# Optimization experiments

Measured on AMD Instinct MI355X. Metric: run time of the kernel, lower is better.

## Reference

```python
import jax, jax.numpy as jnp
import numpy as np

HEADS = 12
NUM_IMS = 1
SCALE = 1.0


def _layernorm(x, g, b, eps=1e-5):
    m = jnp.mean(x, axis=-1, keepdims=True)
    v = jnp.var(x, axis=-1, keepdims=True)
    return (x - m) / jnp.sqrt(v + eps) * g + b


def _mha(q, k, v):
    # q: [B, Nq, C], k/v: [B, Nk, C]; multi-head softmax attention
    B, Nq, C = q.shape
    d = C // HEADS
    qh = q.reshape(B, Nq, HEADS, d)
    kh = k.reshape(B, k.shape[1], HEADS, d)
    vh = v.reshape(B, v.shape[1], HEADS, d)
    sim = jnp.einsum('bihd,bjhd->bhij', qh, kh) * (d ** -0.5)
    w = jax.nn.softmax(sim, axis=-1)
    out = jnp.einsum('bhij,bjhd->bihd', w, vh)
    return out.reshape(B, Nq, C)


def _forward(hidden_states, encoder_hidden_states, ln1_g, ln1_b, ln2_g, ln2_b,
             sa_wq, sa_wk, sa_wv, sa_wo, sa_wo_b, ff_ln_g, ff_ln_b, ff_w1, ff_w2,
             alpha_attn, alpha_dense, ca_wq, ca_wk, ca_wv, ca_wo, ca_wo_b):
    B, N, C = hidden_states.shape
    end_pos = encoder_hidden_states.shape[1] - 16 * NUM_IMS
    text = encoder_hidden_states[:, :end_pos]   # [B, Lt, C]
    face = encoder_hidden_states[:, end_pos:]   # [B, 16, C]

    x = hidden_states
    # gated self-attention over visual tokens + face tokens
    x_ln = _layernorm(x, ln1_g, ln1_b)
    face_ln = _layernorm(face, ln1_g, ln1_b)
    comb = jnp.concatenate([x_ln, face_ln], axis=1)  # [B, N+16, C]
    attn_out = _mha(comb @ sa_wq, comb @ sa_wk, comb @ sa_wv) @ sa_wo + sa_wo_b
    attn_out = attn_out[:, :N]
    x = x + SCALE * jnp.tanh(alpha_attn) * attn_out

    # gated GEGLU feed-forward (norm2 outside, FF has its own LayerNorm)
    h = _layernorm(x, ln2_g, ln2_b)
    h = _layernorm(h, ff_ln_g, ff_ln_b)
    h = h @ ff_w1                                 # [B, N, 2*inner]
    a, gate = jnp.split(h, 2, axis=-1)
    h = (a * jax.nn.gelu(gate, approximate=False)) @ ff_w2
    x = x + SCALE * jnp.tanh(alpha_dense) * h

    residual = x
    # cross attention against text tokens (diffusers Attention, residual_connection=True)
    out = _mha(x @ ca_wq, text @ ca_wk, text @ ca_wv) @ ca_wo + ca_wo_b
    return out + residual


def setup_inputs() -> dict:
    key = jax.random.key(0)
    ks = jax.random.split(key, 16)
    B, N, C, L, INNER = 2, 1024, 768, 77 + 16 * NUM_IMS, 3072
    W = 0.02
    return {
        'hidden_states': jax.random.normal(ks[0], (B, N, C), jnp.float32),
        'encoder_hidden_states': jax.random.normal(ks[1], (B, L, C), jnp.float32),
        'ln1_g': jnp.ones((C,), jnp.float32),
        'ln1_b': jnp.zeros((C,), jnp.float32),
        'ln2_g': jnp.ones((C,), jnp.float32),
        'ln2_b': jnp.zeros((C,), jnp.float32),
        'sa_wq': jax.random.normal(ks[2], (C, C), jnp.float32) * W,
        'sa_wk': jax.random.normal(ks[3], (C, C), jnp.float32) * W,
        'sa_wv': jax.random.normal(ks[4], (C, C), jnp.float32) * W,
        'sa_wo': jax.random.normal(ks[5], (C, C), jnp.float32) * W,
        'sa_wo_b': jnp.zeros((C,), jnp.float32),
        'ff_ln_g': jnp.ones((C,), jnp.float32),
        'ff_ln_b': jnp.zeros((C,), jnp.float32),
        'ff_w1': jax.random.normal(ks[6], (C, 2 * INNER), jnp.float32) * W,
        'ff_w2': jax.random.normal(ks[7], (INNER, C), jnp.float32) * W,
        'alpha_attn': jnp.float32(0.5),
        'alpha_dense': jnp.float32(0.5),
        'ca_wq': jax.random.normal(ks[8], (C, C), jnp.float32) * W,
        'ca_wk': jax.random.normal(ks[9], (C, C), jnp.float32) * W,
        'ca_wv': jax.random.normal(ks[10], (C, C), jnp.float32) * W,
        'ca_wo': jax.random.normal(ks[11], (C, C), jnp.float32) * W,
        'ca_wo_b': jnp.zeros((C,), jnp.float32),
    }


def reference(hidden_states, encoder_hidden_states, ln1_g, ln1_b, ln2_g, ln2_b,
              sa_wq, sa_wk, sa_wv, sa_wo, sa_wo_b, ff_ln_g, ff_ln_b, ff_w1, ff_w2,
              alpha_attn, alpha_dense, ca_wq, ca_wk, ca_wv, ca_wo, ca_wo_b):
    return _forward(hidden_states, encoder_hidden_states, ln1_g, ln1_b, ln2_g, ln2_b,
                    sa_wq, sa_wk, sa_wv, sa_wo, sa_wo_b, ff_ln_g, ff_ln_b, ff_w1, ff_w2,
                    alpha_attn, alpha_dense, ca_wq, ca_wk, ca_wv, ca_wo, ca_wo_b)
```

## Files before the change

kernel.cpp:

```cpp
#include <hip/hip_runtime.h>
#include <hip/hip_bf16.h>
#include <math.h>


#define C_DIM 768
#define B_DIM 2
#define N_DIM 1024
#define NC_DIM 1040
#define L_DIM 93
#define TEXT_LEN 77
#define INNER 3072
#define MNX 1572864

typedef unsigned short ushort_t;
typedef __bf16 bf16x8 __attribute__((ext_vector_type(8)));
typedef float f32x4 __attribute__((ext_vector_type(4)));

__device__ __forceinline__ ushort_t f2b(float f) {
  __hip_bfloat16 h = __float2bfloat16(f);
  return *(ushort_t*)&h;
}
__device__ __forceinline__ float b2f(ushort_t u) {
  __hip_bfloat16 h = *(__hip_bfloat16*)&u;
  return __bfloat162float(h);
}

__device__ __forceinline__ void g2lds16(const void* g, void* l) {
  __builtin_amdgcn_global_load_lds(
      (const __attribute__((address_space(1))) unsigned int*)g,
      (__attribute__((address_space(3))) unsigned int*)l, 16, 0, 0);
}

#define WX1    0u
#define WX2    6291456u
#define WQKV   12582912u
#define WBB1   22167552u
#define WG     47333376u
#define WS1    59916288u
#define WTEXT  63062016u
#define WATT2  63298560u
#define WWQKV  66444288u
#define WWO    69983232u
#define WW1    71162880u
#define WW2    80600064u
#define WCAWQ  85318656u
#define WCAKV  86498304u
#define WCAWO  88857600u
#define WVT1   90037248u
#define WVT2   93379584u
#define WOPART WBB1
#define WLBUF  WG
#define WATTN  (WG + 524288u)
#define WPART  WBB1

__device__ __forceinline__ float block_sum(float v, float* sh) {
#pragma unroll
  for (int o = 32; o > 0; o >>= 1) v += __shfl_down(v, o);
  int lane = threadIdx.x & 63, w = threadIdx.x >> 6;
  if (lane == 0) sh[w] = v;
  __syncthreads();
  float r = sh[0] + sh[1] + sh[2] + sh[3];
  __syncthreads();
  return r;
}

struct WtDesc {
  const float* src[10];
  ushort_t*    dst[10];
  int K[10];
  int N[10];
  int tilesX[10];
  int ileave[10];
  int start[11];
};

__global__ __launch_bounds__(256)
void wtrans_batched(WtDesc d) {
  __shared__ float tile[64][65];
  int bid = blockIdx.x;
  int j = 0;
  while (j < 9 && bid >= d.start[j + 1]) ++j;
  int ti = bid - d.start[j];
  int K = d.K[j], N = d.N[j];
  int n0 = (ti % d.tilesX[j]) * 64, k0 = (ti / d.tilesX[j]) * 64;
  const float* in = d.src[j];
  ushort_t* out = d.dst[j];
  int il = d.ileave[j];
  int t = threadIdx.x;
#pragma unroll
  for (int p = 0; p < 16; ++p) {
    int idx = t + p * 256;
    int r = idx >> 6, c = idx & 63;
    tile[r][c] = in[(size_t)(k0 + r) * N + n0 + c];
  }
  __syncthreads();
#pragma unroll
  for (int p = 0; p < 16; ++p) {
    int idx = t + p * 256;
    int r = idx >> 6, c = idx & 63;
    int nrow = n0 + r;
    int dstrow = il ? ((nrow < INNER) ? (nrow * 2) : ((nrow - INNER) * 2 + 1)) : nrow;
    out[(size_t)dstrow * K + k0 + c] = f2b(tile[c][r]);
  }
}

__global__ __launch_bounds__(256)
void ln_concat_kernel(const float* __restrict__ x, const float* __restrict__ enc,
                      const float* __restrict__ g, const float* __restrict__ b,
                      ushort_t* __restrict__ comb) {
  __shared__ float sh[4];
  int r = blockIdx.x;
  int bb = r / NC_DIM, i = r % NC_DIM;
  const float* src = (i < N_DIM)
      ? (x   + ((size_t)bb * N_DIM + i) * C_DIM)
      : (enc + ((size_t)bb * L_DIM + TEXT_LEN + (i - N_DIM)) * C_DIM);
  float v[3];
#pragma unroll
  for (int j = 0; j < 3; ++j) v[j] = src[threadIdx.x + j * 256];
  float mean = block_sum(v[0] + v[1] + v[2], sh) * (1.f / C_DIM);
  float sq = 0.f;
#pragma unroll
  for (int j = 0; j < 3; ++j) { float d = v[j] - mean; sq += d * d; }
  float rstd = rsqrtf(block_sum(sq, sh) * (1.f / C_DIM) + 1e-5f);
  ushort_t* dst = comb + (size_t)r * C_DIM;
#pragma unroll
  for (int j = 0; j < 3; ++j) {
    int c = threadIdx.x + j * 256;
    dst[c] = f2b((v[j] - mean) * rstd * g[c] + b[c]);
  }
}

__global__ __launch_bounds__(256)
void gemm_bf16(const ushort_t* __restrict__ A, const ushort_t* __restrict__ Bt,
               ushort_t* __restrict__ Ob, ushort_t* __restrict__ Og,
               int M, int N, int K) {
  __shared__ ushort_t sA[2][128 * 32];
  __shared__ ushort_t sB[2][128 * 32];
  int t = threadIdx.x;
  int w = t >> 6, ln = t & 63;
  int m0 = blockIdx.y * 128, n0 = blockIdx.x * 128;
  int wm = (w >> 1) * 64, wn = (w & 1) * 64;
  int lr = ln & 15, lq = ln >> 4;
  int seg_r = ln >> 2, seg_c = (ln & 3) * 8;

  f32x4 acc[4][4];
#pragma unroll
  for (int mi = 0; mi < 4; ++mi)
#pragma unroll
    for (int ni = 0; ni < 4; ++ni) acc[mi][ni] = (f32x4){0.f, 0.f, 0.f, 0.f};

#define STAGE(k0_, buf_)                                                     \
  do {                                                                       \
    _Pragma("unroll") for (int l = 0; l < 2; ++l) {                          \
      int s = w * 2 + l;                                                     \
      int arow = m0 + s * 16 + seg_r;                                        \
      arow = arow < M ? arow : M - 1;                                        \
      g2lds16(A + (size_t)arow * K + (k0_) + seg_c, &sA[buf_][s * 512]);     \
      int nrow = n0 + s * 16 + seg_r;                                        \
      g2lds16(Bt + (size_t)nrow * K + (k0_) + seg_c, &sB[buf_][s * 512]);    \
    }                                                                        \
  } while (0)

  STAGE(0, 0);
  __syncthreads();
  int cur = 0;
  for (int k0 = 0; k0 < K; k0 += 32) {
    if (k0 + 32 < K) STAGE(k0 + 32, cur ^ 1);
    bf16x8 af[4], bfr[4];
#pragma unroll
    for (int mi = 0; mi < 4; ++mi)
      af[mi] = *(const bf16x8*)&sA[cur][(wm + mi * 16 + lr) * 32 + lq * 8];
#pragma unroll
    for (int ni = 0; ni < 4; ++ni)
      bfr[ni] = *(const bf16x8*)&sB[cur][(wn + ni * 16 + lr) * 32 + lq * 8];
#pragma unroll
    for (int mi = 0; mi < 4; ++mi)
#pragma unroll
      for (int ni = 0; ni < 4; ++ni)
        acc[mi][ni] = __builtin_amdgcn_mfma_f32_16x16x32_bf16(
            af[mi], bfr[ni], acc[mi][ni], 0, 0, 0);
    __syncthreads();
    cur ^= 1;
  }
#undef STAGE

  if (Og) {
#pragma unroll
    for (int mi = 0; mi < 4; ++mi)
#pragma unroll
      for (int ni = 0; ni < 4; ++ni) {
        int col = n0 + wn + ni * 16 + lr;
#pragma unroll
        for (int r = 0; r < 4; ++r) {
          float val = acc[mi][ni][r];
          float other = __shfl_xor(val, 1);
          if (!(lr & 1)) {
            float a = val, gate = other;
            float ge = 0.5f * gate * (1.f + erff(gate * 0.70710678118654752f));
            int row = m0 + wm + mi * 16 + lq * 4 + r;
            Og[(size_t)row * INNER + (col >> 1)] = f2b(a * ge);
          }
        }
      }
  } else {
#pragma unroll
    for (int mi = 0; mi < 4; ++mi)
#pragma unroll
      for (int ni = 0; ni < 4; ++ni) {
        int col = n0 + wn + ni * 16 + lr;
#pragma unroll
        for (int r = 0; r < 4; ++r) {
          int row = m0 + wm + mi * 16 + lq * 4 + r;
          if (row < M) Ob[(size_t)row * N + col] = f2b(acc[mi][ni][r]);
        }
      }
  }
}

__global__ __launch_bounds__(256)
void gemm64(const ushort_t* __restrict__ A, const ushort_t* __restrict__ Bt,
            float* __restrict__ Out, ushort_t* __restrict__ Ob,
            float* __restrict__ Part,
            int M, int N, int K, int Ksplit,
            const float* __restrict__ bias, const float* __restrict__ res,
            const float* __restrict__ alphaPtr) {
  __shared__ ushort_t sA[2][4096];
  __shared__ ushort_t sB[2][4096];
  int t = threadIdx.x;
  int w = t >> 6, ln = t & 63;
  int m0 = blockIdx.y * 64, n0 = blockIdx.x * 64;
  int wm = (w >> 1) * 32, wn = (w & 1) * 32;
  int lr = ln & 15, lq = ln >> 4;
  int srow = (w & 1) * 32 + (ln >> 2);
  int skoff = (w >> 1) * 32 + (ln & 3) * 8;
  int kbeg = blockIdx.z * Ksplit;
  int kend = kbeg + Ksplit; if (kend > K) kend = K;

  f32x4 acc[2][2];
#pragma unroll
  for (int mi = 0; mi < 2; ++mi)
#pragma unroll
    for (int ni = 0; ni < 2; ++ni) acc[mi][ni] = (f32x4){0.f, 0.f, 0.f, 0.f};

#define STG64(k0_, buf_)                                                      \
  do {                                                                        \
    _Pragma("unroll") for (int i = 0; i < 2; ++i) {                           \
      int ar = m0 + srow + i * 16; ar = ar < M ? ar : M - 1;                  \
      g2lds16(A + (size_t)ar * K + (k0_) + skoff,                             \
              (char*)sA + (buf_) * 8192 + w * 2048 + i * 1024);               \
      int nr = n0 + srow + i * 16;                                            \
      g2lds16(Bt + (size_t)nr * K + (k0_) + skoff,                            \
              (char*)sB + (buf_) * 8192 + w * 2048 + i * 1024);               \
    }                                                                         \
  } while (0)

  STG64(kbeg, 0);
  __syncthreads();
  int cur = 0;
  for (int k0 = kbeg; k0 < kend; k0 += 64) {
    if (k0 + 64 < kend) STG64(k0 + 64, cur ^ 1);
#pragma unroll
    for (int s = 0; s < 2; ++s) {
      bf16x8 a0 = *(const bf16x8*)&sA[cur][s * 2048 + (wm + lr) * 32 + lq * 8];
      bf16x8 a1 = *(const bf16x8*)&sA[cur][s * 2048 + (wm + 16 + lr) * 32 + lq * 8];
      bf16x8 b0 = *(const bf16x8*)&sB[cur][s * 2048 + (wn + lr) * 32 + lq * 8];
      bf16x8 b1 = *(const bf16x8*)&sB[cur][s * 2048 + (wn + 16 + lr) * 32 + lq * 8];
      acc[0][0] = __builtin_amdgcn_mfma_f32_16x16x32_bf16(a0, b0, acc[0][0], 0, 0, 0);
      acc[0][1] = __builtin_amdgcn_mfma_f32_16x16x32_bf16(a0, b1, acc[0][1], 0, 0, 0);
      acc[1][0] = __builtin_amdgcn_mfma_f32_16x16x32_bf16(a1, b0, acc[1][0], 0, 0, 0);
      acc[1][1] = __builtin_amdgcn_mfma_f32_16x16x32_bf16(a1, b1, acc[1][1], 0, 0, 0);
    }
    __syncthreads();
    cur ^= 1;
  }
#undef STG64

  if (Part) {
    float* P = Part + (size_t)blockIdx.z * M * N;
#pragma unroll
    for (int mi = 0; mi < 2; ++mi)
#pragma unroll
      for (int ni = 0; ni < 2; ++ni) {
        int col = n0 + wn + ni * 16 + lr;
#pragma unroll
        for (int r = 0; r < 4; ++r) {
          int row = m0 + wm + mi * 16 + lq * 4 + r;
          if (row < M) P[(size_t)row * N + col] = acc[mi][ni][r];
        }
      }
  } else {
    float f = alphaPtr ? tanhf(alphaPtr[0]) : 1.0f;
#pragma unroll
    for (int mi = 0; mi < 2; ++mi)
#pragma unroll
      for (int ni = 0; ni < 2; ++ni) {
        int col = n0 + wn + ni * 16 + lr;
        float bv = bias ? bias[col] : 0.f;
#pragma unroll
        for (int r = 0; r < 4; ++r) {
          int row = m0 + wm + mi * 16 + lq * 4 + r;
          if (row < M) {
            float val = acc[mi][ni][r] + bv;
            if (res) val = res[(size_t)row * N + col] + f * val;
            if (Out) Out[(size_t)row * N + col] = val;
            if (Ob)  Ob[(size_t)row * N + col] = f2b(val);
          }
        }
      }
  }
}

__global__ __launch_bounds__(256)
void splitk_epi(const float* __restrict__ Part, int nz, float* __restrict__ Out,
                ushort_t* __restrict__ Ob, int MN, int N,
                const float* __restrict__ bias, const float* __restrict__ res,
                const float* __restrict__ alphaPtr) {
  int idx = (blockIdx.x * 256 + threadIdx.x) * 4;
  if (idx >= MN) return;
  float f = alphaPtr ? tanhf(alphaPtr[0]) : 1.0f;
  float v[4] = {0.f, 0.f, 0.f, 0.f};
  for (int z = 0; z < nz; ++z) {
    float4 a = *(const float4*)&Part[(size_t)z * MN + idx];
    v[0] += a.x; v[1] += a.y; v[2] += a.z; v[3] += a.w;
  }
  if (bias) {
    int col = idx % N;
    float4 bb = *(const float4*)&bias[col];
    v[0] += bb.x; v[1] += bb.y; v[2] += bb.z; v[3] += bb.w;
  }
  if (res) {
    float4 rr = *(const float4*)&res[idx];
    v[0] = rr.x + f * v[0]; v[1] = rr.y + f * v[1];
    v[2] = rr.z + f * v[2]; v[3] = rr.w + f * v[3];
  }
  if (Out) *(float4*)&Out[idx] = make_float4(v[0], v[1], v[2], v[3]);
  if (Ob) {
    ushort4 o;
    o.x = f2b(v[0]); o.y = f2b(v[1]); o.z = f2b(v[2]); o.w = f2b(v[3]);
    *(ushort4*)&Ob[idx] = o;
  }
}

__global__ __launch_bounds__(256)
void woepi_ln_kernel(const float* __restrict__ Part, int nz,
                     const float* __restrict__ bias, const float* __restrict__ xres,
                     const float* __restrict__ alphaPtr, float* __restrict__ x1,
                     const float* __restrict__ g1, const float* __restrict__ b1,
                     const float* __restrict__ g2, const float* __restrict__ b2,
                     ushort_t* __restrict__ hh) {
  __shared__ float sh[4];
  int row = blockIdx.x;
  float f = tanhf(alphaPtr[0]);
  float v[3];
#pragma unroll
  for (int j = 0; j < 3; ++j) {
    int c = threadIdx.x + j * 256;
    float s = 0.f;
    for (int z = 0; z < nz; ++z) s += Part[(size_t)z * MNX + (size_t)row * C_DIM + c];
    s += bias[c];
    float xv = xres[(size_t)row * C_DIM + c] + f * s;
    x1[(size_t)row * C_DIM + c] = xv;
    v[j] = xv;
  }
  float mean = block_sum(v[0] + v[1] + v[2], sh) * (1.f / C_DIM);
  float sq = 0.f;
#pragma unroll
  for (int j = 0; j < 3; ++j) { float d = v[j] - mean; sq += d * d; }
  float rstd = rsqrtf(block_sum(sq, sh) * (1.f / C_DIM) + 1e-5f);
  float y[3];
#pragma unroll
  for (int j = 0; j < 3; ++j) {
    int c = threadIdx.x + j * 256;
    y[j] = (v[j] - mean) * rstd * g1[c] + b1[c];
  }
  float mean2 = block_sum(y[0] + y[1] + y[2], sh) * (1.f / C_DIM);
  sq = 0.f;
#pragma unroll
  for (int j = 0; j < 3; ++j) { float d = y[j] - mean2; sq += d * d; }
  float rstd2 = rsqrtf(block_sum(sq, sh) * (1.f / C_DIM) + 1e-5f);
#pragma unroll
  for (int j = 0; j < 3; ++j) {
    int c = threadIdx.x + j * 256;
    hh[(size_t)row * C_DIM + c] = f2b((y[j] - mean2) * rstd2 * g2[c] + b2[c]);
  }
}

__global__ __launch_bounds__(256)
void vtrans_kernel(const ushort_t* __restrict__ V, ushort_t* __restrict__ Vt,
                   int rows_per_b, int stride, int Nk, int Nkp) {
  __shared__ ushort_t tile[64][68];
  int k0 = blockIdx.x * 64;
  int h = blockIdx.y, b = blockIdx.z;
  int t = threadIdx.x;
#pragma unroll
  for (int p = 0; p < 4; ++p) {
    int r = p * 16 + (t >> 4), c = (t & 15) * 4;
    int key = k0 + r;
    ushort4 u = make_ushort4(0, 0, 0, 0);
    if (key < Nk)
      u = *(const ushort4*)&V[((size_t)(b * rows_per_b + key)) * stride + h * 64 + c];
    *(ushort4*)&tile[r][c] = u;
  }
  __syncthreads();
  size_t base = ((size_t)(b * 12 + h)) * 64 * Nkp;
#pragma unroll
  for (int p = 0; p < 4; ++p) {
    int dv = p * 16 + (t >> 4), kc = (t & 15) * 4;
    ushort4 u;
    u.x = tile[kc + 0][dv]; u.y = tile[kc + 1][dv];
    u.z = tile[kc + 2][dv]; u.w = tile[kc + 3][dv];
    *(ushort4*)&Vt[base + (size_t)dv * Nkp + k0 + kc] = u;
  }
}

__global__ __launch_bounds__(256)
void attn_mfma(const ushort_t* __restrict__ Q, const ushort_t* __restrict__ K,
               const ushort_t* __restrict__ Vt, ushort_t* __restrict__ O,
               float* __restrict__ Opart, float* __restrict__ lbuf,
               int q_rows_per_b, int kv_rows_per_b, int Nk, int Nkp,
               int qstride, int kstride, int nchunk) {
  __shared__ ushort_t sQ[4096];
  __shared__ ushort_t sK[2][4096];
  __shared__ ushort_t sV[2][4096];
  __shared__ ushort_t sP[4][1024];
  const float scale = 0.18033688011112042f;
  const float M0 = 16.0f;
  int t = threadIdx.x;
  int w = t >> 6, ln = t & 63;
  int col = ln & 15, quad = ln >> 4;
  int z = blockIdx.z;
  int b = z / nchunk, kc = z % nchunk;
  int h = blockIdx.y, q0 = blockIdx.x * 64;
  size_t vt_base = ((size_t)(b * 12 + h)) * 64 * Nkp;
  int ntiles = Nkp >> 6;
  int t0 = (kc * ntiles) / nchunk;
  int t1 = ((kc + 1) * ntiles) / nchunk;

#define STAGE_KV(kt_, bb_)                                                    \
  do {                                                                        \
    _Pragma("unroll") for (int s = 0; s < 2; ++s) {                           \
      int key = (kt_) * 64 + w * 16 + (ln >> 2);                              \
      g2lds16(K + (size_t)(b * kv_rows_per_b + key) * kstride                 \
                + h * 64 + s * 32 + (ln & 3) * 8,                             \
              (char*)sK[bb_] + s * 4096 + w * 1024);                          \
      int dv = w * 16 + (ln >> 2);                                            \
      g2lds16(Vt + vt_base + (size_t)dv * Nkp                                 \
                + (kt_) * 64 + s * 32 + (ln & 3) * 8,                         \
              (char*)sV[bb_] + s * 4096 + w * 1024);                          \
    }                                                                         \
  } while (0)

#pragma unroll
  for (int s = 0; s < 2; ++s) {
    int r = q0 + w * 16 + (ln >> 2);
    g2lds16(Q + (size_t)(b * q_rows_per_b + r) * qstride + h * 64 + s * 32 + (ln & 3) * 8,
            (char*)sQ + s * 4096 + w * 1024);
  }
  STAGE_KV(t0, 0);
  __syncthreads();
  bf16x8 qa[2];
#pragma unroll
  for (int s = 0; s < 2; ++s)
    qa[s] = *(const bf16x8*)&sQ[s * 2048 + (w * 16 + col) * 32 + quad * 8];

  f32x4 oacc[4];
#pragma unroll
  for (int i = 0; i < 4; ++i) oacc[i] = (f32x4){0.f, 0.f, 0.f, 0.f};
  float l_i[4] = {0.f, 0.f, 0.f, 0.f};

  ushort_t* sPw = sP[w];
  int bb = 0;

  for (int kt = t0; kt < t1; ++kt) {
    if (kt + 1 < t1) STAGE_KV(kt + 1, bb ^ 1);

    f32x4 cs[4];
#pragma unroll
    for (int nblk = 0; nblk < 4; ++nblk) {
      cs[nblk] = (f32x4){0.f, 0.f, 0.f, 0.f};
#pragma unroll
      for (int s = 0; s < 2; ++s) {
        bf16x8 kb = *(const bf16x8*)&sK[bb][s * 2048 + (nblk * 16 + col) * 32 + quad * 8];
        cs[nblk] = __builtin_amdgcn_mfma_f32_16x16x32_bf16(qa[s], kb, cs[nblk], 0, 0, 0);
      }
    }
    if (kt * 64 + 64 > Nk) {
#pragma unroll
      for (int nblk = 0; nblk < 4; ++nblk) {
        bool valid = (kt * 64 + nblk * 16 + col) < Nk;
#pragma unroll
        for (int r = 0; r < 4; ++r)
          cs[nblk][r] = valid ? cs[nblk][r] : -1e30f;
      }
    }
#pragma unroll
    for (int r = 0; r < 4; ++r) {
      int row = quad * 4 + r;
#pragma unroll
      for (int nblk = 0; nblk < 4; ++nblk) {
        float p = exp2f(fmaf(cs[nblk][r], scale, -M0));
        l_i[r] += p;
        int kin = (nblk & 1) * 16 + col;
        sPw[(nblk >> 1) * 512 + row * 32 + (kin ^ (quad << 3))] = f2b(p);
      }
    }
#pragma unroll
    for (int s = 0; s < 2; ++s) {
      bf16x8 pa = *(const bf16x8*)&sPw[s * 512 + col * 32 + ((quad ^ ((col >> 2) & 3)) << 3)];
#pragma unroll
      for (int nblk = 0; nblk < 4; ++nblk) {
        bf16x8 vb = *(const bf16x8*)&sV[bb][s * 2048 + (nblk * 16 + col) * 32 + quad * 8];
        oacc[nblk] = __builtin_amdgcn_mfma_f32_16x16x32_bf16(pa, vb, oacc[nblk], 0, 0, 0);
      }
    }
    if (kt + 1 < t1) __syncthreads();
    bb ^= 1;
  }
#undef STAGE_KV

#pragma unroll
  for (int r = 0; r < 4; ++r) {
    float ps = l_i[r];
#pragma unroll
    for (int o = 1; o < 16; o <<= 1) ps += __shfl_xor(ps, o);
    int qglob = b * N_DIM + q0 + w * 16 + quad * 4 + r;
    if (Opart) {
      if (col == 0) lbuf[(size_t)kc * (B_DIM * N_DIM * 12) + (size_t)qglob * 12 + h] = ps;
      float* op = Opart + (size_t)kc * MNX + (size_t)qglob * C_DIM + h * 64;
#pragma unroll
      for (int nblk = 0; nblk < 4; ++nblk)
        op[nblk * 16 + col] = oacc[nblk][r];
    } else {
      float inv = 1.f / ps;
#pragma unroll
      for (int nblk = 0; nblk < 4; ++nblk)
        O[(size_t)qglob * C_DIM + h * 64 + nblk * 16 + col] = f2b(oacc[nblk][r] * inv);
    }
  }
}

__global__ __launch_bounds__(256)
void attn_merge(const float* __restrict__ Opart, const float* __restrict__ lbuf,
                ushort_t* __restrict__ Ob, int nchunk) {
  int idx = (blockIdx.x * 256 + threadIdx.x) * 4;
  if (idx >= MNX) return;
  int row = idx / C_DIM, c = idx % C_DIM;
  int h = c >> 6;
  float l = 0.f;
  float v[4] = {0.f, 0.f, 0.f, 0.f};
  for (int kc = 0; kc < nchunk; ++kc) {
    l += lbuf[(size_t)kc * (B_DIM * N_DIM * 12) + (size_t)row * 12 + h];
    float4 p = *(const float4*)&Opart[(size_t)kc * MNX + idx];
    v[0] += p.x; v[1] += p.y; v[2] += p.z; v[3] += p.w;
  }
  float inv = 1.f / l;
  ushort4 o;
  o.x = f2b(v[0] * inv); o.y = f2b(v[1] * inv);
  o.z = f2b(v[2] * inv); o.w = f2b(v[3] * inv);
  *(ushort4*)&Ob[idx] = o;
}

__global__ __launch_bounds__(256)
void gather_text_kernel(const float* __restrict__ enc, ushort_t* __restrict__ out) {
  int r = blockIdx.x;
  int bb = r / TEXT_LEN, j = r % TEXT_LEN;
  const float* src = enc + ((size_t)bb * L_DIM + j) * C_DIM;
  ushort_t* dst = out + (size_t)r * C_DIM;
#pragma unroll
  for (int l = 0; l < 3; ++l) {
    int c = threadIdx.x + l * 256;
    dst[c] = f2b(src[c]);
  }
}

extern "C" void kernel_launch(void* const* d_in, const int* in_sizes, int n_in,
                              void* d_out, int out_size, void* d_ws, size_t ws_size,
                              hipStream_t stream) {
  const float* x        = (const float*)d_in[0];
  const float* enc      = (const float*)d_in[1];
  const float* ln1_g    = (const float*)d_in[2];
  const float* ln1_b    = (const float*)d_in[3];
  const float* ln2_g    = (const float*)d_in[4];
  const float* ln2_b    = (const float*)d_in[5];
  const float* sa_wq    = (const float*)d_in[6];
  const float* sa_wk    = (const float*)d_in[7];
  const float* sa_wv    = (const float*)d_in[8];
  const float* sa_wo    = (const float*)d_in[9];
  const float* sa_wo_b  = (const float*)d_in[10];
  const float* ff_ln_g  = (const float*)d_in[11];
  const float* ff_ln_b  = (const float*)d_in[12];
  const float* ff_w1    = (const float*)d_in[13];
  const float* ff_w2    = (const float*)d_in[14];
  const float* a_attn   = (const float*)d_in[15];
  const float* a_dense  = (const float*)d_in[16];
  const float* ca_wq    = (const float*)d_in[17];
  const float* ca_wk    = (const float*)d_in[18];
  const float* ca_wv    = (const float*)d_in[19];
  const float* ca_wo    = (const float*)d_in[20];
  const float* ca_wo_b  = (const float*)d_in[21];

  char* ws = (char*)d_ws;
  float*    x1     = (float*)(ws + WX1);
  float*    x2     = (float*)(ws + WX2);
  ushort_t* qkv_b  = (ushort_t*)(ws + WQKV);
  ushort_t* q2b    = (ushort_t*)(ws + WQKV);
  ushort_t* kv2b   = (ushort_t*)(ws + WQKV + 3145728u);
  ushort_t* comb_b = (ushort_t*)(ws + WBB1);
  float*    opart  = (float*)(ws + WOPART);
  float*    lbuf   = (float*)(ws + WLBUF);
  ushort_t* attn_b = (ushort_t*)(ws + WATTN);
  ushort_t* g_b    = (ushort_t*)(ws + WG);
  ushort_t* hh     = (ushort_t*)(ws + WS1);
  ushort_t* x2b    = (ushort_t*)(ws + WS1);
  ushort_t* text_b = (ushort_t*)(ws + WTEXT);
  ushort_t* attn2b = (ushort_t*)(ws + WATT2);
  ushort_t* wqkv_t = (ushort_t*)(ws + WWQKV);
  ushort_t* wo_t   = (ushort_t*)(ws + WWO);
  ushort_t* w1_t   = (ushort_t*)(ws + WW1);
  ushort_t* w2_t   = (ushort_t*)(ws + WW2);
  ushort_t* cawq_t = (ushort_t*)(ws + WCAWQ);
  ushort_t* cakv_t = (ushort_t*)(ws + WCAKV);
  ushort_t* cawo_t = (ushort_t*)(ws + WCAWO);
  ushort_t* vt1    = (ushort_t*)(ws + WVT1);
  ushort_t* vt2    = (ushort_t*)(ws + WVT2);
  float* part = (float*)(ws + WPART);
  float* out = (float*)d_out;

  const int Mc = B_DIM * NC_DIM;
  const int Mx = B_DIM * N_DIM;
  const int Mt = B_DIM * TEXT_LEN;

  WtDesc wd;
  const float* srcs[10] = {sa_wq, sa_wk, sa_wv, sa_wo, ca_wq, ca_wk, ca_wv, ca_wo, ff_w1, ff_w2};
  ushort_t* dsts[10] = {wqkv_t, wqkv_t + 589824, wqkv_t + 2 * 589824, wo_t,
                        cawq_t, cakv_t, cakv_t + 589824, cawo_t, w1_t, w2_t};
  int Ks[10] = {768, 768, 768, 768, 768, 768, 768, 768, 768, 3072};
  int Ns[10] = {768, 768, 768, 768, 768, 768, 768, 768, 6144, 768};
  int total = 0;
  for (int j = 0; j < 10; ++j) {
    wd.src[j] = srcs[j]; wd.dst[j] = dsts[j];
    wd.K[j] = Ks[j]; wd.N[j] = Ns[j];
    wd.tilesX[j] = Ns[j] / 64;
    wd.ileave[j] = (j == 8) ? 1 : 0;
    wd.start[j] = total;
    total += (Ns[j] / 64) * (Ks[j] / 64);
  }
  wd.start[10] = total;

  wtrans_batched<<<total, 256, 0, stream>>>(wd);
  ln_concat_kernel<<<Mc, 256, 0, stream>>>(x, enc, ln1_g, ln1_b, comb_b);
  gemm64<<<dim3(36, 33, 1), 256, 0, stream>>>(
      comb_b, wqkv_t, nullptr, qkv_b, nullptr, Mc, 2304, 768, 768,
      nullptr, nullptr, nullptr);
  vtrans_kernel<<<dim3(17, 12, B_DIM), 256, 0, stream>>>(
      qkv_b + 1536, vt1, NC_DIM, 2304, NC_DIM, 1088);
  attn_mfma<<<dim3(N_DIM / 64, 12, B_DIM * 4), 256, 0, stream>>>(
      qkv_b + 0, qkv_b + 768, vt1, nullptr, opart, lbuf,
      NC_DIM, NC_DIM, NC_DIM, 1088, 2304, 2304, 4);
  attn_merge<<<MNX / 1024, 256, 0, stream>>>(opart, lbuf, attn_b, 4);
  gemm64<<<dim3(12, 32, 2), 256, 0, stream>>>(
      attn_b, wo_t, nullptr, nullptr, part, Mx, 768, 768, 384,
      nullptr, nullptr, nullptr);
  woepi_ln_kernel<<<Mx, 256, 0, stream>>>(
      part, 2, sa_wo_b, x, a_attn, x1, ln2_g, ln2_b, ff_ln_g, ff_ln_b, hh);
  gemm_bf16<<<dim3(48, 16), 256, 0, stream>>>(
      hh, w1_t, nullptr, g_b, Mx, 6144, 768);
  gemm64<<<dim3(12, 32, 4), 256, 0, stream>>>(
      g_b, w2_t, nullptr, nullptr, part, Mx, 768, 3072, 768,
      nullptr, nullptr, nullptr);
  splitk_epi<<<MNX / 1024, 256, 0, stream>>>(
      part, 4, x2, x2b, MNX, 768, nullptr, x1, a_dense);
  gather_text_kernel<<<Mt, 256, 0, stream>>>(enc, text_b);
  gemm64<<<dim3(12, 32, 2), 256, 0, stream>>>(
      x2b, cawq_t, nullptr, nullptr, part, Mx, 768, 768, 384,
      nullptr, nullptr, nullptr);
  splitk_epi<<<MNX / 1024, 256, 0, stream>>>(
      part, 2, nullptr, q2b, MNX, 768, nullptr, nullptr, nullptr);
  gemm64<<<dim3(24, 3, 1), 256, 0, stream>>>(
      text_b, cakv_t, nullptr, kv2b, nullptr, Mt, 1536, 768, 768,
      nullptr, nullptr, nullptr);
  vtrans_kernel<<<dim3(2, 12, B_DIM), 256, 0, stream>>>(
      kv2b + 768, vt2, TEXT_LEN, 1536, TEXT_LEN, 128);
  attn_mfma<<<dim3(N_DIM / 64, 12, B_DIM), 256, 0, stream>>>(
      q2b, kv2b + 0, vt2, attn2b, nullptr, nullptr,
      N_DIM, TEXT_LEN, TEXT_LEN, 128, 768, 1536, 1);
  gemm64<<<dim3(12, 32, 2), 256, 0, stream>>>(
      attn2b, cawo_t, nullptr, nullptr, part, Mx, 768, 768, 384,
      nullptr, nullptr, nullptr);
  splitk_epi<<<MNX / 1024, 256, 0, stream>>>(
      part, 2, out, nullptr, MNX, 768, ca_wo_b, x2, nullptr);
}
```

Baseline: 326.6 us.

## Replace FF1 GEGLU GEMM with 256x256-tile, 8-wave pipelined kernel

```diff
diff --git a/kernel.cpp b/kernel.cpp
--- a/kernel.cpp
+++ b/kernel.cpp
@@ -130,91 +130,123 @@
   }
 }
 
-__global__ __launch_bounds__(256)
-void gemm_bf16(const ushort_t* __restrict__ A, const ushort_t* __restrict__ Bt,
-               ushort_t* __restrict__ Ob, ushort_t* __restrict__ Og,
-               int M, int N, int K) {
-  __shared__ ushort_t sA[2][128 * 32];
-  __shared__ ushort_t sB[2][128 * 32];
-  int t = threadIdx.x;
-  int w = t >> 6, ln = t & 63;
-  int m0 = blockIdx.y * 128, n0 = blockIdx.x * 128;
-  int wm = (w >> 1) * 64, wn = (w & 1) * 64;
-  int lr = ln & 15, lq = ln >> 4;
-  int seg_r = ln >> 2, seg_c = (ln & 3) * 8;
-
-  f32x4 acc[4][4];
-#pragma unroll
-  for (int mi = 0; mi < 4; ++mi)
+__global__ __launch_bounds__(512, 2)
+void gemm256_geglu(const ushort_t* __restrict__ A, const ushort_t* __restrict__ Bt,
+                   ushort_t* __restrict__ Og, int K) {
+  __shared__ ushort_t lds[8][8192];
+  const int t = threadIdx.x;
+  const int w = t >> 6, ln = t & 63;
+  const int lr = ln & 15, lq = ln >> 4;
+  const int wr = w >> 2, wc = w & 3;
+  const int m0 = blockIdx.y * 256, n0 = blockIdx.x * 256;
+  const ushort_t* Ab = A + (size_t)m0 * K;
+  const ushort_t* Bb = Bt + (size_t)n0 * K;
+
+  const int srow = t >> 2;
+  const int scol = ((t & 3) ^ ((srow >> 1) & 3)) * 8;
+  const int fsw = (lr >> 1) & 3;
+
+#define STG(tile_, mat_, kh_)                                                \
+  do {                                                                       \
+    const ushort_t* gb_ = (mat_) ? Bb : Ab;                                  \
+    int slot_ = (((tile_) & 1) << 2) | ((mat_) << 1) | (kh_);                \
+    int kb_ = (tile_) * 64 + (kh_) * 32;                                     \
+    g2lds16(gb_ + (size_t)srow * K + kb_ + scol, &lds[slot_][w * 512]);      \
+    g2lds16(gb_ + (size_t)(srow + 128) * K + kb_ + scol,                     \
+            &lds[slot_][4096 + w * 512]);                                    \
+  } while (0)
+
+#define LDA(kh_, mi_)                                                        \
+  (*(const bf16x8*)&lds[(buf << 2) | (kh_)]                                  \
+        [(wr * 128 + (mi_) * 16 + lr) * 32 + ((lq ^ fsw) << 3)])
+#define LDB(kh_, ni_)                                                        \
+  (*(const bf16x8*)&lds[(buf << 2) | 2 | (kh_)]                              \
+        [(wc * 64 + (ni_) * 16 + lr) * 32 + ((lq ^ fsw) << 3)])
+
+#define BAR() asm volatile("s_barrier" ::: "memory")
+#define WAITV(n_) asm volatile("s_waitcnt vmcnt(" #n_ ")" ::: "memory")
+#define MFMA16(j0_, j1_)                                                     \
+  do {                                                                       \
+    __builtin_amdgcn_s_setprio(1);                                           \
+    _Pragma("unroll") for (int mi = 0; mi < 8; ++mi) {                       \
+      acc[mi][j0_] = __builtin_amdgcn_mfma_f32_16x16x32_bf16(                \
+          a[mi], b0, acc[mi][j0_], 0, 0, 0);                                 \
+      acc[mi][j1_] = __builtin_amdgcn_mfma_f32_16x16x32_bf16(                \
+          a[mi], b1, acc[mi][j1_], 0, 0, 0);                                 \
+    }                                                                        \
+    __builtin_amdgcn_s_setprio(0);                                           \
+  } while (0)
+
+  f32x4 acc[8][4];
+#pragma unroll
+  for (int mi = 0; mi < 8; ++mi)
 #pragma unroll
     for (int ni = 0; ni < 4; ++ni) acc[mi][ni] = (f32x4){0.f, 0.f, 0.f, 0.f};
 
-#define STAGE(k0_, buf_)                                                     \
-  do {                                                                       \
-    _Pragma("unroll") for (int l = 0; l < 2; ++l) {                          \
-      int s = w * 2 + l;                                                     \
-      int arow = m0 + s * 16 + seg_r;                                        \
-      arow = arow < M ? arow : M - 1;                                        \
-      g2lds16(A + (size_t)arow * K + (k0_) + seg_c, &sA[buf_][s * 512]);     \
-      int nrow = n0 + s * 16 + seg_r;                                        \
-      g2lds16(Bt + (size_t)nrow * K + (k0_) + seg_c, &sB[buf_][s * 512]);    \
-    }                                                                        \
-  } while (0)
-
-  STAGE(0, 0);
-  __syncthreads();
-  int cur = 0;
-  for (int k0 = 0; k0 < K; k0 += 32) {
-    if (k0 + 32 < K) STAGE(k0 + 32, cur ^ 1);
-    bf16x8 af[4], bfr[4];
-#pragma unroll
-    for (int mi = 0; mi < 4; ++mi)
-      af[mi] = *(const bf16x8*)&sA[cur][(wm + mi * 16 + lr) * 32 + lq * 8];
-#pragma unroll
-    for (int ni = 0; ni < 4; ++ni)
-      bfr[ni] = *(const bf16x8*)&sB[cur][(wn + ni * 16 + lr) * 32 + lq * 8];
-#pragma unroll
-    for (int mi = 0; mi < 4; ++mi)
-#pragma unroll
-      for (int ni = 0; ni < 4; ++ni)
-        acc[mi][ni] = __builtin_amdgcn_mfma_f32_16x16x32_bf16(
-            af[mi], bfr[ni], acc[mi][ni], 0, 0, 0);
-    __syncthreads();
-    cur ^= 1;
-  }
-#undef STAGE
-
-  if (Og) {
-#pragma unroll
-    for (int mi = 0; mi < 4; ++mi)
-#pragma unroll
-      for (int ni = 0; ni < 4; ++ni) {
-        int col = n0 + wn + ni * 16 + lr;
-#pragma unroll
-        for (int r = 0; r < 4; ++r) {
-          float val = acc[mi][ni][r];
-          float other = __shfl_xor(val, 1);
-          if (!(lr & 1)) {
-            float a = val, gate = other;
-            float ge = 0.5f * gate * (1.f + erff(gate * 0.70710678118654752f));
-            int row = m0 + wm + mi * 16 + lq * 4 + r;
-            Og[(size_t)row * INNER + (col >> 1)] = f2b(a * ge);
-          }
+  STG(0, 0, 0); STG(0, 1, 0); STG(0, 0, 1); STG(0, 1, 1);
+  STG(1, 0, 0); STG(1, 1, 0);
+  WAITV(4);
+  BAR();
+
+  const int NT = K >> 6;
+  for (int tt = 0; tt < NT; ++tt) {
+    const int buf = tt & 1;
+    bf16x8 a[8], b0, b1;
+
+#pragma unroll
+    for (int mi = 0; mi < 8; ++mi) a[mi] = LDA(0, mi);
+    b0 = LDB(0, 0); b1 = LDB(0, 1);
+    if (tt + 1 < NT) STG(tt + 1, 0, 1);
+    BAR();
+    MFMA16(0, 1);
+    BAR();
+
+    b0 = LDB(0, 2); b1 = LDB(0, 3);
+    if (tt + 1 < NT) STG(tt + 1, 1, 1);
+    BAR();
+    MFMA16(2, 3);
+    WAITV(8);
+    BAR();
+
+#pragma unroll
+    for (int mi = 0; mi < 8; ++mi) a[mi] = LDA(1, mi);
+    b0 = LDB(1, 0); b1 = LDB(1, 1);
+    if (tt + 2 < NT) STG(tt + 2, 0, 0);
+    BAR();
+    MFMA16(0, 1);
+    BAR();
+
+    b0 = LDB(1, 2); b1 = LDB(1, 3);
+    if (tt + 2 < NT) STG(tt + 2, 1, 0);
+    BAR();
+    MFMA16(2, 3);
+    if (tt + 2 < NT) { WAITV(4); } else { WAITV(0); }
+    BAR();
+  }
+#undef STG
+#undef LDA
+#undef LDB
+#undef BAR
+#undef WAITV
+#undef MFMA16
+
+#pragma unroll
+  for (int mi = 0; mi < 8; ++mi)
+#pragma unroll
+    for (int ni = 0; ni < 4; ++ni) {
+      int col = n0 + wc * 64 + ni * 16 + lr;
+#pragma unroll
+      for (int r = 0; r < 4; ++r) {
+        float val = acc[mi][ni][r];
+        float other = __shfl_xor(val, 1);
+        if (!(lr & 1)) {
+          float aa = val, gate = other;
+          float ge = 0.5f * gate * (1.f + erff(gate * 0.70710678118654752f));
+          int row = m0 + wr * 128 + mi * 16 + lq * 4 + r;
+          Og[(size_t)row * INNER + (col >> 1)] = f2b(aa * ge);
         }
       }
-  } else {
-#pragma unroll
-    for (int mi = 0; mi < 4; ++mi)
-#pragma unroll
-      for (int ni = 0; ni < 4; ++ni) {
-        int col = n0 + wn + ni * 16 + lr;
-#pragma unroll
-        for (int r = 0; r < 4; ++r) {
-          int row = m0 + wm + mi * 16 + lq * 4 + r;
-          if (row < M) Ob[(size_t)row * N + col] = f2b(acc[mi][ni][r]);
-        }
-      }
-  }
+    }
 }
 
 __global__ __launch_bounds__(256)
@@ -663,8 +695,7 @@
       nullptr, nullptr, nullptr);
   woepi_ln_kernel<<<Mx, 256, 0, stream>>>(
       part, 2, sa_wo_b, x, a_attn, x1, ln2_g, ln2_b, ff_ln_g, ff_ln_b, hh);
-  gemm_bf16<<<dim3(48, 16), 256, 0, stream>>>(
-      hh, w1_t, nullptr, g_b, Mx, 6144, 768);
+  gemm256_geglu<<<dim3(24, 8), 512, 0, stream>>>(hh, w1_t, g_b, 768);
   gemm64<<<dim3(12, 32, 4), 256, 0, stream>>>(
       g_b, w2_t, nullptr, nullptr, part, Mx, 768, 3072, 768,
       nullptr, nullptr, nullptr);
```

Result: slower. 392.6 us (+20.2%).
